# Kernel tuning notes

Hardware: AMD Instinct MI355X
Metric: run time of the kernel (lower is better)

Reference implementation:

```python
import jax, jax.numpy as jnp
import numpy as np

H = W = 28
PI = np.pi


def _encoder(x, c1w, c1b, c2w, c2b):
    dn = ('NCHW', 'OIHW', 'NCHW')
    h = jax.lax.conv_general_dilated(x, c1w, (1, 1), 'SAME', dimension_numbers=dn)
    h = jax.nn.relu(h + c1b[None, :, None, None])
    h = jax.lax.conv_general_dilated(h, c2w, (2, 2), 'SAME', dimension_numbers=dn)
    return jax.nn.relu(h + c2b[None, :, None, None])


def _angles_deg(x):
    # Batched replacement of the per-image masked-point PCA loop:
    # masked 2x2 covariance + closed-form top eigenvector (same math as
    # torch.svd of the mean-centered selected points).
    B = x.shape[0]
    imgs = x.reshape(B, -1)                       # [B, 784]
    m = (imgs > 0.5).astype(x.dtype)              # boolean selection as weights
    xs = jnp.linspace(-14.0, 14.0, 28)
    ys = jnp.linspace(14.0, -14.0, 28)
    gx, gy = jnp.meshgrid(xs, ys)                 # 'xy' indexing, matches np.meshgrid
    gx = gx.reshape(-1)
    gy = gy.reshape(-1)                           # [784]
    n = jnp.maximum(m.sum(1), 1.0)                # [B]
    mx = (m * gx).sum(1) / n
    my = (m * gy).sum(1) / n
    dx = gx[None, :] - mx[:, None]                # [B, 784]
    dy = gy[None, :] - my[:, None]
    a = (m * dx * dx).sum(1)                      # unnormalized covariance entries
    b = (m * dx * dy).sum(1)
    c = (m * dy * dy).sum(1)
    lam = 0.5 * (a + c) + jnp.sqrt(0.25 * (a - c) ** 2 + b * b)  # top eigenvalue
    v1 = jnp.stack([b, lam - a], -1)              # two algebraic eigenvector forms
    v2 = jnp.stack([lam - c, b], -1)
    use1 = (v1 * v1).sum(-1) >= (v2 * v2).sum(-1)
    v = jnp.where(use1[:, None], v1, v2)
    v = jnp.where((v * v).sum(-1, keepdims=True) < 1e-12,
                  jnp.array([1.0, 0.0], dtype=x.dtype), v)  # isotropic fallback
    return jnp.arctan2(v[:, 1], v[:, 0]) * (180.0 / PI)


def _rotate(x, angles_deg):
    # kornia.geometry.rotate: rotate by angle degrees (CCW) about image center,
    # bilinear interpolation, zero padding. x: [B,1,H,W].
    B = x.shape[0]
    th = angles_deg * (PI / 180.0)
    cs = jnp.cos(th)[:, None, None]
    sn = jnp.sin(th)[:, None, None]
    yy, xx = jnp.meshgrid(jnp.arange(H, dtype=x.dtype),
                          jnp.arange(W, dtype=x.dtype), indexing='ij')
    cx = (W - 1) / 2.0
    cy = (H - 1) / 2.0
    dxp = xx - cx
    dyp = yy - cy
    # inverse warp (OpenCV getRotationMatrix2D convention)
    sx = cs * dxp + sn * dyp + cx                 # [B,H,W] source coords
    sy = -sn * dxp + cs * dyp + cy
    x0 = jnp.floor(sx)
    y0 = jnp.floor(sy)
    wx1 = sx - x0
    wx0 = 1.0 - wx1
    wy1 = sy - y0
    wy0 = 1.0 - wy1
    img = x.reshape(B, -1)                        # single channel

    def samp(yi, xi):
        valid = (xi >= 0) & (xi <= W - 1) & (yi >= 0) & (yi <= H - 1)
        xi_ = jnp.clip(xi, 0, W - 1).astype(jnp.int32)
        yi_ = jnp.clip(yi, 0, H - 1).astype(jnp.int32)
        idx = (yi_ * W + xi_).reshape(B, -1)
        vals = jnp.take_along_axis(img, idx, axis=1).reshape(B, H, W)
        return vals * valid.astype(x.dtype)

    out = (samp(y0, x0) * wy0 * wx0 + samp(y0, x0 + 1) * wy0 * wx1 +
           samp(y0 + 1, x0) * wy1 * wx0 + samp(y0 + 1, x0 + 1) * wy1 * wx1)
    return out[:, None, :, :]


def setup_inputs() -> dict:
    key = jax.random.key(0)
    ks = jax.random.split(key, 5)
    B = 2048
    x = jax.random.uniform(ks[0], (B, 1, 28, 28), jnp.float32)
    conv1_w = jax.random.normal(ks[1], (32, 1, 3, 3), jnp.float32) * 0.1
    conv1_b = jnp.zeros((32,), jnp.float32)
    conv2_w = jax.random.normal(ks[2], (64, 32, 3, 3), jnp.float32) * 0.05
    conv2_b = jnp.zeros((64,), jnp.float32)
    pred_w = jax.random.normal(ks[3], (64 * 14 * 14, 10), jnp.float32) * 0.01
    pred_b = jnp.zeros((10,), jnp.float32)
    return {'x': x, 'conv1_w': conv1_w, 'conv1_b': conv1_b,
            'conv2_w': conv2_w, 'conv2_b': conv2_b,
            'pred_w': pred_w, 'pred_b': pred_b}


def reference(x, conv1_w, conv1_b, conv2_w, conv2_b, pred_w, pred_b):
    angles = jax.lax.stop_gradient(_angles_deg(x))  # original detaches angles
    x_canonized = _rotate(x, -angles)
    reps = _encoder(x_canonized, conv1_w, conv1_b, conv2_w, conv2_b)
    reps = reps.reshape(x.shape[0], -1)             # [B, 12544]
    return reps @ pred_w + pred_b                   # [B, 10]
```

## Files before the change

### kernel.cpp

```cpp
#include <hip/hip_runtime.h>
#include <math.h>

typedef __attribute__((ext_vector_type(8))) short short8;
typedef __attribute__((ext_vector_type(4))) float f32x4;
typedef __attribute__((ext_vector_type(8))) _Float16 half8;
typedef __attribute__((ext_vector_type(4))) _Float16 half4;
typedef __attribute__((ext_vector_type(2))) _Float16 half2v;
typedef __attribute__((ext_vector_type(4))) unsigned int uint4v;

#define H1_OFF   3840
#define H1_ROWB  1920
#define LDS_BYTES (H1_OFF + 29*H1_ROWB)
#define RED_OFF  25344

__device__ __forceinline__ int h1_byte(int y, int x, int chunk) {
    int b = H1_OFF + y*H1_ROWB + x*64 + chunk*16;
    return b ^ (((x >> 1) & 7) << 4);
}

__device__ __forceinline__ half2v hmax2(half2v a) {
#if defined(__has_builtin) && __has_builtin(__builtin_elementwise_max)
    half2v z = {(_Float16)0.0f, (_Float16)0.0f};
    return __builtin_elementwise_max(a, z);
#else
    half2v r;
    r[0] = a[0] > (_Float16)0.0f ? a[0] : (_Float16)0.0f;
    r[1] = a[1] > (_Float16)0.0f ? a[1] : (_Float16)0.0f;
    return r;
#endif
}

__global__ __launch_bounds__(256) void prep_kernel(
    const float* __restrict__ w1, const float* __restrict__ b1,
    const float* __restrict__ w2, const float* __restrict__ pw,
    unsigned* __restrict__ w1pk,
    unsigned short* __restrict__ w2frag, unsigned short* __restrict__ pwt2)
{
    const int NW1 = 160;
    const int NW2 = 9*4*64*8;
    const int NPW = 10*12544;
    for (int idx = blockIdx.x*256 + threadIdx.x; idx < NW1 + NW2 + NPW; idx += gridDim.x*256) {
        if (idx < NW1) {
            half2v h;
            if (idx < 144) {
                int c2 = idx / 9, k = idx - 9*c2;
                h[0] = (_Float16)w1[(2*c2)*9 + k];
                h[1] = (_Float16)w1[(2*c2+1)*9 + k];
            } else {
                int c2 = idx - 144;
                h[0] = (_Float16)b1[2*c2];
                h[1] = (_Float16)b1[2*c2+1];
            }
            w1pk[idx] = __builtin_bit_cast(unsigned, h);
        } else if (idx < NW1 + NW2) {
            int d = idx - NW1;
            int m = d & 7;
            int l = (d >> 3) & 63;
            int f = d >> 9;
            int oct = f & 3;
            int kk = f >> 2;
            int oc = oct*16 + (l & 15);
            int c  = (l >> 4)*8 + m;
            _Float16 h = (_Float16)w2[(oc*32 + c)*9 + kk];
            w2frag[d] = __builtin_bit_cast(unsigned short, h);
        } else {
            int j = idx - NW1 - NW2;
            int k = j / 12544;
            int i2 = j - k*12544;
            _Float16 h = (_Float16)pw[i2*10 + k];
            pwt2[k*12544 + i2] = __builtin_bit_cast(unsigned short, h);
        }
    }
}

__global__ __launch_bounds__(256) void angle_kernel(
    const float* __restrict__ x, float2* __restrict__ csn)
{
    const int b = blockIdx.x;
    const int t = threadIdx.x;
    const float* xb = x + b * 784;

    double S = 0, Sx = 0, Sy = 0, Sxx = 0, Sxy = 0, Syy = 0;
    for (int p = t; p < 784; p += 256) {
        float v = xb[p];
        if (v > 0.5f) {
            int j = p / 28;
            int i = p - j * 28;
            double gx = -14.0 + i * (28.0 / 27.0);
            double gy =  14.0 - j * (28.0 / 27.0);
            S   += 1.0;
            Sx  += gx;   Sy  += gy;
            Sxx += gx * gx; Sxy += gx * gy; Syy += gy * gy;
        }
    }
    #pragma unroll
    for (int off = 32; off; off >>= 1) {
        S   += __shfl_down(S, off);
        Sx  += __shfl_down(Sx, off);
        Sy  += __shfl_down(Sy, off);
        Sxx += __shfl_down(Sxx, off);
        Sxy += __shfl_down(Sxy, off);
        Syy += __shfl_down(Syy, off);
    }
    __shared__ double red[4][6];
    const int lane = t & 63, w = t >> 6;
    if (lane == 0) {
        red[w][0] = S; red[w][1] = Sx; red[w][2] = Sy;
        red[w][3] = Sxx; red[w][4] = Sxy; red[w][5] = Syy;
    }
    __syncthreads();
    if (t == 0) {
        S   = red[0][0] + red[1][0] + red[2][0] + red[3][0];
        Sx  = red[0][1] + red[1][1] + red[2][1] + red[3][1];
        Sy  = red[0][2] + red[1][2] + red[2][2] + red[3][2];
        Sxx = red[0][3] + red[1][3] + red[2][3] + red[3][3];
        Sxy = red[0][4] + red[1][4] + red[2][4] + red[3][4];
        Syy = red[0][5] + red[1][5] + red[2][5] + red[3][5];

        double n  = (S < 1.0) ? 1.0 : S;
        double mx = Sx / n, my = Sy / n;
        double a  = Sxx - 2.0 * mx * Sx + mx * mx * S;
        double bb = Sxy - mx * Sy - my * Sx + mx * my * S;
        double cc = Syy - 2.0 * my * Sy + my * my * S;
        double lam = 0.5 * (a + cc) + sqrt(0.25 * (a - cc) * (a - cc) + bb * bb);
        double v1x = bb, v1y = lam - a;
        double v2x = lam - cc, v2y = bb;
        double n1 = v1x * v1x + v1y * v1y;
        double n2 = v2x * v2x + v2y * v2y;
        double vx, vy;
        if (n1 >= n2) { vx = v1x; vy = v1y; } else { vx = v2x; vy = v2y; }
        if (vx * vx + vy * vy < 1e-12) { vx = 1.0; vy = 0.0; }
        double th = -atan2(vy, vx);
        csn[b] = make_float2((float)cos(th), (float)sin(th));
    }
}

__global__ __launch_bounds__(1024, 8) void fused_kernel(
    const float* __restrict__ x,
    const unsigned* __restrict__ w1pk,
    const float* __restrict__ b2,
    const unsigned short* __restrict__ w2frag,
    const unsigned short* __restrict__ pwt2,
    const float* __restrict__ pb,
    const float2* __restrict__ csn,
    float* __restrict__ out)
{
    __shared__ __align__(16) char lds[LDS_BYTES];
    float* rotf = (float*)lds;
    float* imgf = (float*)(lds + H1_OFF);
    _Float16* reps16 = (_Float16*)lds;
    float* red  = (float*)(lds + RED_OFF);

    const int b = blockIdx.x;
    const int t = threadIdx.x;
    const int lane = t & 63;
    const int wv = t >> 6;
    const int l15 = lane & 15;
    const int g   = lane >> 4;

    const float* xb = x + b*784;
    int ty = t/28, tx = t - ty*28;
    if (t < 784) {
        imgf[ty*32 + tx] = xb[t];
    }
    if (t < 960) rotf[t] = 0.0f;
    __syncthreads();

    if (t < 784) {
        const float2 cn = csn[b];
        const float cs = cn.x, sn = cn.y;
        float dxp = (float)tx - 13.5f;
        float dyp = (float)ty - 13.5f;
        float sx =  cs*dxp + sn*dyp + 13.5f;
        float sy = -sn*dxp + cs*dyp + 13.5f;
        float x0 = floorf(sx), y0 = floorf(sy);
        float wx1 = sx - x0, wx0 = 1.0f - wx1;
        float wy1 = sy - y0, wy0 = 1.0f - wy1;
        int ix0 = (int)x0, iy0 = (int)y0;
        int ix1 = ix0 + 1, iy1 = iy0 + 1;
        int cx0 = min(max(ix0, 0), 27), cy0 = min(max(iy0, 0), 27);
        int cx1 = min(max(ix1, 0), 27), cy1 = min(max(iy1, 0), 27);
        bool vx0 = (ix0 >= 0) & (ix0 <= 27);
        bool vx1 = (ix1 >= 0) & (ix1 <= 27);
        bool vy0 = (iy0 >= 0) & (iy0 <= 27);
        bool vy1 = (iy1 >= 0) & (iy1 <= 27);
        float a00 = imgf[cy0*32 + cx0];
        float a01 = imgf[cy0*32 + cx1];
        float a10 = imgf[cy1*32 + cx0];
        float a11 = imgf[cy1*32 + cx1];
        float v00 = (vx0 & vy0) ? a00 : 0.f;
        float v01 = (vx1 & vy0) ? a01 : 0.f;
        float v10 = (vx0 & vy1) ? a10 : 0.f;
        float v11 = (vx1 & vy1) ? a11 : 0.f;
        float r = v00*wy0*wx0 + v01*wy0*wx1 + v10*wy1*wx0 + v11*wy1*wx1;
        rotf[(ty + 1)*32 + (tx + 1)] = r;
    }
    __syncthreads();

    if (t < 228) {
        short8 z8 = {0,0,0,0,0,0,0,0};
        int cell = t >> 2;
        int chunk = t & 3;
        int y, xx;
        if (cell < 29) { y = 28; xx = cell; } else { y = cell - 29; xx = 28; }
        *(short8*)(lds + h1_byte(y, xx, chunk)) = z8;
    }

    if (lane < 49) {
        int p = wv*49 + lane;
        int py = p/28, px = p - py*28;
        const float* rp = rotf + py*32 + px;
        half2v rs[9];
        {
            float rv[9] = { rp[0],  rp[1],  rp[2],
                            rp[32], rp[33], rp[34],
                            rp[64], rp[65], rp[66] };
            #pragma unroll
            for (int m = 0; m < 9; ++m) {
                _Float16 h = (_Float16)rv[m];
                rs[m][0] = h; rs[m][1] = h;
            }
        }
        half2v acc2[16];
        #pragma unroll
        for (int c2 = 0; c2 < 16; ++c2) {
            half2v a = __builtin_bit_cast(half2v, w1pk[144 + c2]);
            #pragma unroll
            for (int k = 0; k < 9; ++k) {
                half2v w = __builtin_bit_cast(half2v, w1pk[c2*9 + k]);
                a = w * rs[k] + a;
            }
            acc2[c2] = hmax2(a);
        }
        #pragma unroll
        for (int c8 = 0; c8 < 4; ++c8) {
            uint4v vh;
            #pragma unroll
            for (int j = 0; j < 4; ++j)
                vh[j] = __builtin_bit_cast(unsigned, acc2[c8*4 + j]);
            *(uint4v*)(lds + h1_byte(py, px, c8)) = vh;
        }
    }
    __syncthreads();

    const int oct = wv & 3;
    const int trow = wv >> 2;
    const int nq = (trow == 0) ? 4 : 3;
    int oyq[4], oxq[4];
    #pragma unroll
    for (int q = 0; q < 4; ++q) {
        int sp = (trow + 4*q)*16 + l15;
        sp = sp > 195 ? 195 : sp;
        oyq[q] = sp/14;
        oxq[q] = sp - 14*oyq[q];
    }
    f32x4 acc[4];
    #pragma unroll
    for (int q = 0; q < 4; ++q) acc[q] = (f32x4){0.f, 0.f, 0.f, 0.f};

    for (int kk = 0; kk < 9; ++kk) {
        int ky = kk/3;
        int kx = kk - ky*3;
        half8 bh = *(const half8*)(w2frag + (kk*4 + oct)*512 + lane*8);
        #pragma unroll
        for (int q = 0; q < 4; ++q) {
            if (q < nq) {
                int y = 2*oyq[q] + ky, xx = 2*oxq[q] + kx;
                half8 ah = *(const half8*)(lds + h1_byte(y, xx, g));
                acc[q] = __builtin_amdgcn_mfma_f32_16x16x32_f16(ah, bh, acc[q], 0, 0, 0);
            }
        }
    }
    __syncthreads();

    {
        int oc = oct*16 + l15;
        float bias = b2[oc];
        #pragma unroll
        for (int q = 0; q < 4; ++q) {
            if (q < nq) {
                int sp0 = (trow + 4*q)*16 + 4*g;
                if (sp0 + 3 < 196) {
                    half4 v;
                    #pragma unroll
                    for (int j = 0; j < 4; ++j)
                        v[j] = (_Float16)fmaxf(acc[q][j] + bias, 0.0f);
                    *(half4*)(reps16 + oc*196 + sp0) = v;
                }
            }
        }
    }
    __syncthreads();

    float a10[10];
    #pragma unroll
    for (int k = 0; k < 10; ++k) a10[k] = 0.0f;
    const unsigned* pw32 = (const unsigned*)pwt2;
    const unsigned* rp32 = (const unsigned*)reps16;
    for (int ip = t; ip < 6272; ip += 1024) {
        unsigned rv = rp32[ip];
#if defined(__has_builtin) && __has_builtin(__builtin_amdgcn_fdot2)
        half2v rh = __builtin_bit_cast(half2v, rv);
        #pragma unroll
        for (int k = 0; k < 10; ++k) {
            half2v ph = __builtin_bit_cast(half2v, pw32[k*6272 + ip]);
            a10[k] = __builtin_amdgcn_fdot2(rh, ph, a10[k], false);
        }
#else
        half2v rh = __builtin_bit_cast(half2v, rv);
        float r0 = (float)rh[0], r1 = (float)rh[1];
        #pragma unroll
        for (int k = 0; k < 10; ++k) {
            half2v ph = __builtin_bit_cast(half2v, pw32[k*6272 + ip]);
            a10[k] = fmaf(r0, (float)ph[0], fmaf(r1, (float)ph[1], a10[k]));
        }
#endif
    }
    #pragma unroll
    for (int k = 0; k < 10; ++k) {
        float v = a10[k];
        #pragma unroll
        for (int off = 32; off; off >>= 1) v += __shfl_down(v, off);
        a10[k] = v;
    }
    if (lane == 0) {
        #pragma unroll
        for (int k = 0; k < 10; ++k) red[wv*10 + k] = a10[k];
    }
    __syncthreads();
    if (t < 10) {
        float s = pb[t];
        #pragma unroll
        for (int w = 0; w < 16; ++w) s += red[w*10 + t];
        out[b*10 + t] = s;
    }
}

extern "C" void kernel_launch(void* const* d_in, const int* in_sizes, int n_in,
                              void* d_out, int out_size, void* d_ws, size_t ws_size,
                              hipStream_t stream)
{
    const float* x   = (const float*)d_in[0];
    const float* w1  = (const float*)d_in[1];
    const float* b1  = (const float*)d_in[2];
    const float* w2  = (const float*)d_in[3];
    const float* b2  = (const float*)d_in[4];
    const float* pw  = (const float*)d_in[5];
    const float* pb  = (const float*)d_in[6];
    float* out = (float*)d_out;

    const int B = in_sizes[0] / 784;

    char* wsb = (char*)d_ws;
    float2* csn = (float2*)wsb;
    unsigned* w1pk = (unsigned*)(wsb + (size_t)B*8);
    unsigned short* w2frag = (unsigned short*)(wsb + (size_t)B*8 + 640);
    unsigned short* pwt2   = (unsigned short*)(wsb + (size_t)B*8 + 640 + 36864);

    prep_kernel<<<563, 256, 0, stream>>>(w1, b1, w2, pw, w1pk, w2frag, pwt2);
    angle_kernel<<<B, 256, 0, stream>>>(x, csn);
    fused_kernel<<<B, 1024, 0, stream>>>(x, w1pk, b2, w2frag, pwt2, pb, csn, out);
}
```

Measured before the change: 81.79 us.

## Merge prep and angle kernels, hoist conv2 weight fragments, unroll head loop

Merges the weight-prep and angle kernels into one launch, giving the first 64 blocks the prep work and the remaining blocks the per-image angles. This removes one kernel launch and its dependency gap. It also preloads all nine conv2 B fragments into registers before the MFMA loop and fully unrolls that loop. The linear head loop is unrolled into six full iterations plus a tail. The costs are more register use, and the prep work now runs on fewer blocks.

```diff
diff --git a/kernel.cpp b/kernel.cpp
--- a/kernel.cpp
+++ b/kernel.cpp
@@ -12,6 +12,8 @@
 #define H1_ROWB  1920
 #define LDS_BYTES (H1_OFF + 29*H1_ROWB)
 #define RED_OFF  25344
+
+#define PREP_BLOCKS 64
 
 __device__ __forceinline__ int h1_byte(int y, int x, int chunk) {
     int b = H1_OFF + y*H1_ROWB + x*64 + chunk*16;
@@ -30,54 +32,57 @@
 #endif
 }
 
-__global__ __launch_bounds__(256) void prep_kernel(
+__global__ __launch_bounds__(256) void prep_angle_kernel(
     const float* __restrict__ w1, const float* __restrict__ b1,
     const float* __restrict__ w2, const float* __restrict__ pw,
+    const float* __restrict__ x,
     unsigned* __restrict__ w1pk,
-    unsigned short* __restrict__ w2frag, unsigned short* __restrict__ pwt2)
+    unsigned short* __restrict__ w2frag, unsigned short* __restrict__ pwt2,
+    float2* __restrict__ csn)
 {
-    const int NW1 = 160;
-    const int NW2 = 9*4*64*8;
-    const int NPW = 10*12544;
-    for (int idx = blockIdx.x*256 + threadIdx.x; idx < NW1 + NW2 + NPW; idx += gridDim.x*256) {
-        if (idx < NW1) {
-            half2v h;
-            if (idx < 144) {
-                int c2 = idx / 9, k = idx - 9*c2;
-                h[0] = (_Float16)w1[(2*c2)*9 + k];
-                h[1] = (_Float16)w1[(2*c2+1)*9 + k];
+    __shared__ double red[4][6];
+    const int t = threadIdx.x;
+
+    if (blockIdx.x < PREP_BLOCKS) {
+        const int NW1 = 160;
+        const int NW2 = 9*4*64*8;
+        const int NPW = 10*12544;
+        for (int idx = blockIdx.x*256 + t; idx < NW1 + NW2 + NPW; idx += PREP_BLOCKS*256) {
+            if (idx < NW1) {
+                half2v h;
+                if (idx < 144) {
+                    int c2 = idx / 9, k = idx - 9*c2;
+                    h[0] = (_Float16)w1[(2*c2)*9 + k];
+                    h[1] = (_Float16)w1[(2*c2+1)*9 + k];
+                } else {
+                    int c2 = idx - 144;
+                    h[0] = (_Float16)b1[2*c2];
+                    h[1] = (_Float16)b1[2*c2+1];
+                }
+                w1pk[idx] = __builtin_bit_cast(unsigned, h);
+            } else if (idx < NW1 + NW2) {
+                int d = idx - NW1;
+                int m = d & 7;
+                int l = (d >> 3) & 63;
+                int f = d >> 9;
+                int oct = f & 3;
+                int kk = f >> 2;
+                int oc = oct*16 + (l & 15);
+                int c  = (l >> 4)*8 + m;
+                _Float16 h = (_Float16)w2[(oc*32 + c)*9 + kk];
+                w2frag[d] = __builtin_bit_cast(unsigned short, h);
             } else {
-                int c2 = idx - 144;
-                h[0] = (_Float16)b1[2*c2];
-                h[1] = (_Float16)b1[2*c2+1];
-            }
-            w1pk[idx] = __builtin_bit_cast(unsigned, h);
-        } else if (idx < NW1 + NW2) {
-            int d = idx - NW1;
-            int m = d & 7;
-            int l = (d >> 3) & 63;
-            int f = d >> 9;
-            int oct = f & 3;
-            int kk = f >> 2;
-            int oc = oct*16 + (l & 15);
-            int c  = (l >> 4)*8 + m;
-            _Float16 h = (_Float16)w2[(oc*32 + c)*9 + kk];
-            w2frag[d] = __builtin_bit_cast(unsigned short, h);
-        } else {
-            int j = idx - NW1 - NW2;
-            int k = j / 12544;
-            int i2 = j - k*12544;
-            _Float16 h = (_Float16)pw[i2*10 + k];
-            pwt2[k*12544 + i2] = __builtin_bit_cast(unsigned short, h);
-        }
-    }
-}
-
-__global__ __launch_bounds__(256) void angle_kernel(
-    const float* __restrict__ x, float2* __restrict__ csn)
-{
-    const int b = blockIdx.x;
-    const int t = threadIdx.x;
+                int j = idx - NW1 - NW2;
+                int k = j / 12544;
+                int i2 = j - k*12544;
+                _Float16 h = (_Float16)pw[i2*10 + k];
+                pwt2[k*12544 + i2] = __builtin_bit_cast(unsigned short, h);
+            }
+        }
+        return;
+    }
+
+    const int b = blockIdx.x - PREP_BLOCKS;
     const float* xb = x + b * 784;
 
     double S = 0, Sx = 0, Sy = 0, Sxx = 0, Sxy = 0, Syy = 0;
@@ -102,7 +107,6 @@
         Sxy += __shfl_down(Sxy, off);
         Syy += __shfl_down(Syy, off);
     }
-    __shared__ double red[4][6];
     const int lane = t & 63, w = t >> 6;
     if (lane == 0) {
         red[w][0] = S; red[w][1] = Sx; red[w][2] = Sy;
@@ -254,20 +258,25 @@
         oyq[q] = sp/14;
         oxq[q] = sp - 14*oyq[q];
     }
+    half8 bhr[9];
+    #pragma unroll
+    for (int kk = 0; kk < 9; ++kk)
+        bhr[kk] = *(const half8*)(w2frag + (kk*4 + oct)*512 + lane*8);
+
     f32x4 acc[4];
     #pragma unroll
     for (int q = 0; q < 4; ++q) acc[q] = (f32x4){0.f, 0.f, 0.f, 0.f};
 
+    #pragma unroll
     for (int kk = 0; kk < 9; ++kk) {
-        int ky = kk/3;
-        int kx = kk - ky*3;
-        half8 bh = *(const half8*)(w2frag + (kk*4 + oct)*512 + lane*8);
+        const int ky = kk/3;
+        const int kx = kk - ky*3;
         #pragma unroll
         for (int q = 0; q < 4; ++q) {
             if (q < nq) {
                 int y = 2*oyq[q] + ky, xx = 2*oxq[q] + kx;
                 half8 ah = *(const half8*)(lds + h1_byte(y, xx, g));
-                acc[q] = __builtin_amdgcn_mfma_f32_16x16x32_f16(ah, bh, acc[q], 0, 0, 0);
+                acc[q] = __builtin_amdgcn_mfma_f32_16x16x32_f16(ah, bhr[kk], acc[q], 0, 0, 0);
             }
         }
     }
@@ -297,7 +306,29 @@
     for (int k = 0; k < 10; ++k) a10[k] = 0.0f;
     const unsigned* pw32 = (const unsigned*)pwt2;
     const unsigned* rp32 = (const unsigned*)reps16;
-    for (int ip = t; ip < 6272; ip += 1024) {
+    #pragma unroll
+    for (int j = 0; j < 6; ++j) {
+        int ip = t + j*1024;
+        unsigned rv = rp32[ip];
+#if defined(__has_builtin) && __has_builtin(__builtin_amdgcn_fdot2)
+        half2v rh = __builtin_bit_cast(half2v, rv);
+        #pragma unroll
+        for (int k = 0; k < 10; ++k) {
+            half2v ph = __builtin_bit_cast(half2v, pw32[k*6272 + ip]);
+            a10[k] = __builtin_amdgcn_fdot2(rh, ph, a10[k], false);
+        }
+#else
+        half2v rh = __builtin_bit_cast(half2v, rv);
+        float r0 = (float)rh[0], r1 = (float)rh[1];
+        #pragma unroll
+        for (int k = 0; k < 10; ++k) {
+            half2v ph = __builtin_bit_cast(half2v, pw32[k*6272 + ip]);
+            a10[k] = fmaf(r0, (float)ph[0], fmaf(r1, (float)ph[1], a10[k]));
+        }
+#endif
+    }
+    if (t < 128) {
+        int ip = t + 6144;
         unsigned rv = rp32[ip];
 #if defined(__has_builtin) && __has_builtin(__builtin_amdgcn_fdot2)
         half2v rh = __builtin_bit_cast(half2v, rv);
@@ -357,7 +388,7 @@
     unsigned short* w2frag = (unsigned short*)(wsb + (size_t)B*8 + 640);
     unsigned short* pwt2   = (unsigned short*)(wsb + (size_t)B*8 + 640 + 36864);
 
-    prep_kernel<<<563, 256, 0, stream>>>(w1, b1, w2, pw, w1pk, w2frag, pwt2);
-    angle_kernel<<<B, 256, 0, stream>>>(x, csn);
+    prep_angle_kernel<<<PREP_BLOCKS + B, 256, 0, stream>>>(
+        w1, b1, w2, pw, x, w1pk, w2frag, pwt2, csn);
     fused_kernel<<<B, 1024, 0, stream>>>(x, w1pk, b2, w2frag, pwt2, pb, csn, out);
 }
```

Result: slower. 99.88 us (+22.1%).
